# Kernel optimization log

Measured on AMD Instinct MI355X. Metric: run time of the kernel, lower is better.

Reference implementation:

```python
import jax, jax.numpy as jnp
import numpy as np

B, T, D, DH, DFF = 4, 2048, 1024, 1024, 4096


def setup_inputs() -> dict:
    key = jax.random.key(0)
    ks = jax.random.split(key, 8)
    s = 0.02
    return {
        "x": jax.random.normal(ks[0], (B, T, D), jnp.float32),
        "ln1_g": jnp.ones((D,), jnp.float32),
        "ln1_b": jnp.zeros((D,), jnp.float32),
        "W_q": jax.random.normal(ks[1], (D, DH), jnp.float32) * s,
        "b_q": jnp.zeros((DH,), jnp.float32),
        "W_k": jax.random.normal(ks[2], (D, DH), jnp.float32) * s,
        "b_k": jnp.zeros((DH,), jnp.float32),
        "W_v": jax.random.normal(ks[3], (D, DH), jnp.float32) * s,
        "b_v": jnp.zeros((DH,), jnp.float32),
        "ln2_g": jnp.ones((D,), jnp.float32),
        "ln2_b": jnp.zeros((D,), jnp.float32),
        "W_in": jax.random.normal(ks[4], (D, DFF), jnp.float32) * s,
        "b_in": jnp.zeros((DFF,), jnp.float32),
        "W_out": jax.random.normal(ks[5], (DFF, D), jnp.float32) * s,
        "b_out": jnp.zeros((D,), jnp.float32),
    }


def _layernorm(x, g, b, eps=1e-5):
    mu = jnp.mean(x, axis=-1, keepdims=True)
    var = jnp.var(x, axis=-1, keepdims=True)
    return (x - mu) * jax.lax.rsqrt(var + eps) * g + b


def reference(x, ln1_g, ln1_b, W_q, b_q, W_k, b_k, W_v, b_v,
              ln2_g, ln2_b, W_in, b_in, W_out, b_out):
    # --- attention branch (pre-LN) ---
    h = _layernorm(x, ln1_g, ln1_b)                      # [B,T,D]
    Q = h @ W_q + b_q                                    # [B,T,DH]
    K = h @ W_k + b_k
    V = h @ W_v + b_v
    scale = 1.0 / jnp.sqrt(jnp.asarray(K.shape[-1], h.dtype))
    att = jnp.einsum("btd,bsd->bts", Q, K) * scale       # [B,T,T]
    # NOTE: source calls att.masked_fill(...) without assignment -> mask
    # is discarded; faithfully no causal mask applied here.
    att = jax.nn.softmax(att, axis=-1)
    attn_out = jnp.einsum("bts,bsd->btd", att, V)        # [B,T,DH]
    x = x + attn_out
    # --- MLP branch (pre-LN) ---
    h2 = _layernorm(x, ln2_g, ln2_b)
    ff = jax.nn.gelu(h2 @ W_in + b_in, approximate=False)
    x = x + (ff @ W_out + b_out)
    return x
```

## Files before the change

### kernel.cpp

```cpp
#include <hip/hip_runtime.h>
#include <hip/hip_bf16.h>

#define B_    4
#define T_    2048
#define D_    1024
#define DH_   1024
#define DFF_  4096
#define MTOT  (B_ * T_)

using f32x4  = __attribute__((ext_vector_type(4))) float;
using bf16x8 = __attribute__((ext_vector_type(8))) short;

__device__ __forceinline__ unsigned short f2bf(float f) {
    unsigned u = __builtin_bit_cast(unsigned, f);
    u += 0x7fffu + ((u >> 16) & 1u);
    return (unsigned short)(u >> 16);
}

__device__ __forceinline__ void gload16(const short* g, short* l) {
    __builtin_amdgcn_global_load_lds(
        (const __attribute__((address_space(1))) unsigned int*)g,
        (__attribute__((address_space(3))) unsigned int*)l, 16, 0, 0);
}

__global__ __launch_bounds__(256) void transp_f32_bf16(
    const float* __restrict__ src, short* __restrict__ dst, int K, int N) {
    __shared__ float tile[32][33];
    int tk = blockIdx.y * 32, tn = blockIdx.x * 32;
    int tx = threadIdx.x & 31, ty = threadIdx.x >> 5;
#pragma unroll
    for (int i = 0; i < 4; i++) {
        int r = ty + i * 8;
        tile[r][tx] = src[(size_t)(tk + r) * N + tn + tx];
    }
    __syncthreads();
#pragma unroll
    for (int i = 0; i < 4; i++) {
        int r = ty + i * 8;
        dst[(size_t)(tn + r) * K + tk + tx] = f2bf(tile[tx][r]);
    }
}

__global__ void copyv(const float* __restrict__ s, float* __restrict__ d, int n) {
    int i = blockIdx.x * blockDim.x + threadIdx.x;
    if (i < n) d[i] = s[i];
}

__global__ __launch_bounds__(256) void ln_rows(
    const float* __restrict__ x, const float* __restrict__ g,
    const float* __restrict__ bta, short* __restrict__ out) {
    int row = blockIdx.x;
    const float* xr = x + (size_t)row * D_;
    int t = threadIdx.x;
    float4 v = *(const float4*)(xr + t * 4);
    float s  = v.x + v.y + v.z + v.w;
    float s2 = v.x * v.x + v.y * v.y + v.z * v.z + v.w * v.w;
#pragma unroll
    for (int off = 1; off < 64; off <<= 1) {
        s  += __shfl_xor(s, off);
        s2 += __shfl_xor(s2, off);
    }
    __shared__ float as_[4], as2_[4];
    int wave = t >> 6, lane = t & 63;
    if (lane == 0) { as_[wave] = s; as2_[wave] = s2; }
    __syncthreads();
    s  = as_[0] + as_[1] + as_[2] + as_[3];
    s2 = as2_[0] + as2_[1] + as2_[2] + as2_[3];
    float mean = s * (1.0f / D_);
    float var  = s2 * (1.0f / D_) - mean * mean;
    float rstd = rsqrtf(var + 1e-5f);
    float4 gv = *(const float4*)(g + t * 4);
    float4 bv = *(const float4*)(bta + t * 4);
    short4 o;
    o.x = f2bf((v.x - mean) * rstd * gv.x + bv.x);
    o.y = f2bf((v.y - mean) * rstd * gv.y + bv.y);
    o.z = f2bf((v.z - mean) * rstd * gv.z + bv.z);
    o.w = f2bf((v.w - mean) * rstd * gv.w + bv.w);
    *(short4*)(out + (size_t)row * D_ + t * 4) = o;
}

__global__ __launch_bounds__(256) void softmax_rows(float* __restrict__ S) {
    size_t row = blockIdx.x;
    float* sr = S + row * (size_t)T_;
    int t = threadIdx.x;
    float4 v0 = *(const float4*)(sr + t * 4);
    float4 v1 = *(const float4*)(sr + 1024 + t * 4);
    const float c = 0.03125f;
    float vv[8] = {v0.x * c, v0.y * c, v0.z * c, v0.w * c,
                   v1.x * c, v1.y * c, v1.z * c, v1.w * c};
    float mx = -1e30f;
#pragma unroll
    for (int i = 0; i < 8; i++) mx = fmaxf(mx, vv[i]);
#pragma unroll
    for (int off = 1; off < 64; off <<= 1) mx = fmaxf(mx, __shfl_xor(mx, off));
    __shared__ float sm_[4], ss[4];
    int wave = t >> 6, lane = t & 63;
    if (lane == 0) sm_[wave] = mx;
    __syncthreads();
    mx = fmaxf(fmaxf(sm_[0], sm_[1]), fmaxf(sm_[2], sm_[3]));
    float sum = 0.f;
#pragma unroll
    for (int i = 0; i < 8; i++) { vv[i] = expf(vv[i] - mx); sum += vv[i]; }
#pragma unroll
    for (int off = 1; off < 64; off <<= 1) sum += __shfl_xor(sum, off);
    if (lane == 0) ss[wave] = sum;
    __syncthreads();
    sum = ss[0] + ss[1] + ss[2] + ss[3];
    float inv = 1.0f / sum;
    short* pr = (short*)sr;
    short4 oa, ob;
    oa.x = f2bf(vv[0] * inv); oa.y = f2bf(vv[1] * inv);
    oa.z = f2bf(vv[2] * inv); oa.w = f2bf(vv[3] * inv);
    ob.x = f2bf(vv[4] * inv); ob.y = f2bf(vv[5] * inv);
    ob.z = f2bf(vv[6] * inv); ob.w = f2bf(vv[7] * inv);
    *(short4*)(pr + t * 4) = oa;
    *(short4*)(pr + 1024 + t * 4) = ob;
}

#define SLOT 8192
template<int BIAS_MODE, int ACT, int RES, int OUT_BF16>
__global__ __launch_bounds__(512, 2) void gemm8(
    const short* __restrict__ A, int lda, long long sA,
    const short* __restrict__ Bt, int ldb, long long sB,
    void* __restrict__ C, int ldc, long long sC,
    const float* __restrict__ bias,
    const float* __restrict__ res, int ldr, long long sR,
    int K) {
    extern __shared__ short smem_[];
    short* shA = smem_;
    short* shB = smem_ + 4 * SLOT;
    int z = blockIdx.z;
    int bm = blockIdx.y * 256, bn = blockIdx.x * 256;
    const short* gA = A  + (size_t)z * sA + (size_t)bm * lda;
    const short* gB = Bt + (size_t)z * sB + (size_t)bn * ldb;
    int tid = threadIdx.x, lane = tid & 63, w = tid >> 6;
    int wr = w >> 2, wc = w & 3;

    const short *pA0, *pA1, *pB0, *pB1;
    short *ldA0 = nullptr, *ldA1 = nullptr, *ldB0 = nullptr, *ldB1 = nullptr;
    {
        int o0 = tid * 16, o1 = (512 + tid) * 16;
        int s0 = o0 ^ (((o0 >> 7) & 3) << 4);
        int s1 = o1 ^ (((o1 >> 7) & 3) << 4);
        int r0 = s0 >> 6, c0 = (s0 & 63) >> 1;
        int r1 = s1 >> 6, c1 = (s1 & 63) >> 1;
        pA0 = gA + (size_t)r0 * lda + c0;
        pA1 = gA + (size_t)r1 * lda + c1;
        pB0 = gB + (size_t)r0 * ldb + c0;
        pB1 = gB + (size_t)r1 * ldb + c1;
        ldA0 = shA + tid * 8; ldA1 = shA + 4096 + tid * 8;
        ldB0 = shB + tid * 8; ldB1 = shB + 4096 + tid * 8;
    }
    int aoff[8], boff[4];
#pragma unroll
    for (int f = 0; f < 8; f++) {
        int b = (wr * 128 + f * 16 + (lane & 15)) * 64 + (lane >> 4) * 16;
        aoff[f] = b ^ (((b >> 7) & 3) << 4);
    }
#pragma unroll
    for (int f = 0; f < 4; f++) {
        int b = (wc * 64 + f * 16 + (lane & 15)) * 64 + (lane >> 4) * 16;
        boff[f] = b ^ (((b >> 7) & 3) << 4);
    }

    int nk = K >> 5;
    f32x4 acc[8][4] = {};

    gload16(pA0,      ldA0);          gload16(pA1,      ldA1);
    gload16(pB0,      ldB0);          gload16(pB1,      ldB1);
    gload16(pA0 + 32, ldA0 + SLOT);   gload16(pA1 + 32, ldA1 + SLOT);
    gload16(pB0 + 32, ldB0 + SLOT);   gload16(pB1 + 32, ldB1 + SLOT);
    asm volatile("s_waitcnt vmcnt(4)" ::: "memory");
    __builtin_amdgcn_s_barrier();

    for (int t = 0; t < nk; t++) {
        const char* sA_ = (const char*)(shA + (t & 3) * SLOT);
        const char* sB_ = (const char*)(shB + (t & 3) * SLOT);
        int e  = (t + 2) & 3;
        int ks = (t + 2 < nk ? t + 2 : nk - 1) * 32;
        bf16x8 a0 = *(const bf16x8*)(sA_ + aoff[0]);
        bf16x8 a1 = *(const bf16x8*)(sA_ + aoff[1]);
        bf16x8 a2 = *(const bf16x8*)(sA_ + aoff[2]);
        bf16x8 a3 = *(const bf16x8*)(sA_ + aoff[3]);
        bf16x8 b0 = *(const bf16x8*)(sB_ + boff[0]);
        bf16x8 b1 = *(const bf16x8*)(sB_ + boff[1]);
        bf16x8 b2 = *(const bf16x8*)(sB_ + boff[2]);
        bf16x8 b3 = *(const bf16x8*)(sB_ + boff[3]);
        gload16(pA0 + ks, shA + e * SLOT + tid * 8);
        gload16(pA1 + ks, shA + e * SLOT + 4096 + tid * 8);
        __builtin_amdgcn_s_barrier();
        asm volatile("s_waitcnt lgkmcnt(0)" ::: "memory");
        __builtin_amdgcn_sched_barrier(0);
        __builtin_amdgcn_s_setprio(1);
#define MF(r, av) \
        acc[r][0] = __builtin_amdgcn_mfma_f32_16x16x32_bf16(av, b0, acc[r][0], 0, 0, 0); \
        acc[r][1] = __builtin_amdgcn_mfma_f32_16x16x32_bf16(av, b1, acc[r][1], 0, 0, 0); \
        acc[r][2] = __builtin_amdgcn_mfma_f32_16x16x32_bf16(av, b2, acc[r][2], 0, 0, 0); \
        acc[r][3] = __builtin_amdgcn_mfma_f32_16x16x32_bf16(av, b3, acc[r][3], 0, 0, 0);
        MF(0, a0) MF(1, a1) MF(2, a2) MF(3, a3)
        __builtin_amdgcn_s_setprio(0);
        __builtin_amdgcn_s_barrier();
        a0 = *(const bf16x8*)(sA_ + aoff[4]);
        a1 = *(const bf16x8*)(sA_ + aoff[5]);
        a2 = *(const bf16x8*)(sA_ + aoff[6]);
        a3 = *(const bf16x8*)(sA_ + aoff[7]);
        gload16(pB0 + ks, shB + e * SLOT + tid * 8);
        gload16(pB1 + ks, shB + e * SLOT + 4096 + tid * 8);
        asm volatile("s_waitcnt vmcnt(4)" ::: "memory");
        __builtin_amdgcn_s_barrier();
        asm volatile("s_waitcnt lgkmcnt(0)" ::: "memory");
        __builtin_amdgcn_sched_barrier(0);
        __builtin_amdgcn_s_setprio(1);
        MF(4, a0) MF(5, a1) MF(6, a2) MF(7, a3)
#undef MF
        __builtin_amdgcn_s_setprio(0);
        __builtin_amdgcn_s_barrier();
    }
    asm volatile("s_waitcnt vmcnt(0)" ::: "memory");

    size_t zc = (size_t)z * (size_t)sC;
#pragma unroll
    for (int fr = 0; fr < 8; fr++) {
#pragma unroll
        for (int fn = 0; fn < 4; fn++) {
            int col = bn + wc * 64 + fn * 16 + (lane & 15);
#pragma unroll
            for (int r = 0; r < 4; r++) {
                int row = bm + wr * 128 + fr * 16 + (lane >> 4) * 4 + r;
                float v = acc[fr][fn][r];
                if (BIAS_MODE == 1) v += bias[col];
                else if (BIAS_MODE == 2) v += bias[row];
                if (ACT == 1) v = 0.5f * v * (1.0f + erff(v * 0.70710678118654752f));
                if (RES) v += res[(size_t)z * sR + (size_t)row * ldr + col];
                if (OUT_BF16) ((short*)C)[zc + (size_t)row * ldc + col] = f2bf(v);
                else          ((float*)C)[zc + (size_t)row * ldc + col] = v;
            }
        }
    }
}

#define SHBYTES (8 * SLOT * 2)

extern "C" void kernel_launch(void* const* d_in, const int* in_sizes, int n_in,
                              void* d_out, int out_size, void* d_ws, size_t ws_size,
                              hipStream_t stream) {
    const float* x    = (const float*)d_in[0];
    const float* ln1g = (const float*)d_in[1];
    const float* ln1b = (const float*)d_in[2];
    const float* Wq   = (const float*)d_in[3];
    const float* bq   = (const float*)d_in[4];
    const float* Wk   = (const float*)d_in[5];
    const float* bk   = (const float*)d_in[6];
    const float* Wv   = (const float*)d_in[7];
    const float* bv   = (const float*)d_in[8];
    const float* ln2g = (const float*)d_in[9];
    const float* ln2b = (const float*)d_in[10];
    const float* Win  = (const float*)d_in[11];
    const float* bin  = (const float*)d_in[12];
    const float* Wout = (const float*)d_in[13];
    const float* bout = (const float*)d_in[14];

    char* ws = (char*)d_ws;
    size_t off = 0;
    auto alloc = [&](size_t bytes) {
        void* p = ws + off;
        off += (bytes + 255) & ~(size_t)255;
        return p;
    };
    short* WqkT  = (short*)alloc((size_t)2048 * 1024 * 2);
    short* WvT   = (short*)alloc((size_t)1024 * 1024 * 2);
    short* WinT  = (short*)alloc((size_t)4096 * 1024 * 2);
    short* WoutT = (short*)alloc((size_t)1024 * 4096 * 2);
    float* bqk   = (float*)alloc((size_t)2048 * 4);
    short* h     = (short*)alloc((size_t)MTOT * 1024 * 2);
    short* QK    = (short*)alloc((size_t)MTOT * 2048 * 2);
    short* VT    = (short*)alloc((size_t)1024 * 8192 * 2);
    float* S     = (float*)alloc((size_t)4 * 2048 * 2048 * 4);
    float* x1    = (float*)alloc((size_t)MTOT * 1024 * 4);
    (void)ws_size; (void)in_sizes; (void)n_in; (void)out_size;

    hipFuncSetAttribute((const void*)gemm8<1,0,0,1>, hipFuncAttributeMaxDynamicSharedMemorySize, SHBYTES);
    hipFuncSetAttribute((const void*)gemm8<2,0,0,1>, hipFuncAttributeMaxDynamicSharedMemorySize, SHBYTES);
    hipFuncSetAttribute((const void*)gemm8<0,0,0,0>, hipFuncAttributeMaxDynamicSharedMemorySize, SHBYTES);
    hipFuncSetAttribute((const void*)gemm8<0,0,1,0>, hipFuncAttributeMaxDynamicSharedMemorySize, SHBYTES);
    hipFuncSetAttribute((const void*)gemm8<1,1,0,1>, hipFuncAttributeMaxDynamicSharedMemorySize, SHBYTES);
    hipFuncSetAttribute((const void*)gemm8<1,0,1,0>, hipFuncAttributeMaxDynamicSharedMemorySize, SHBYTES);

    transp_f32_bf16<<<dim3(32, 32), 256, 0, stream>>>(Wq, WqkT, 1024, 1024);
    transp_f32_bf16<<<dim3(32, 32), 256, 0, stream>>>(Wk, WqkT + (size_t)1024 * 1024, 1024, 1024);
    transp_f32_bf16<<<dim3(32, 32), 256, 0, stream>>>(Wv, WvT, 1024, 1024);
    transp_f32_bf16<<<dim3(128, 32), 256, 0, stream>>>(Win, WinT, 1024, 4096);
    transp_f32_bf16<<<dim3(32, 128), 256, 0, stream>>>(Wout, WoutT, 4096, 1024);
    copyv<<<4, 256, 0, stream>>>(bq, bqk, 1024);
    copyv<<<4, 256, 0, stream>>>(bk, bqk + 1024, 1024);

    ln_rows<<<MTOT, 256, 0, stream>>>(x, ln1g, ln1b, h);

    gemm8<1, 0, 0, 1><<<dim3(8, 32, 1), 512, SHBYTES, stream>>>(
        h, 1024, 0, WqkT, 1024, 0, QK, 2048, 0, bqk, nullptr, 0, 0, 1024);

    gemm8<2, 0, 0, 1><<<dim3(32, 4, 1), 512, SHBYTES, stream>>>(
        WvT, 1024, 0, h, 1024, 0, VT, 8192, 0, bv, nullptr, 0, 0, 1024);

    gemm8<0, 0, 0, 0><<<dim3(8, 8, 4), 512, SHBYTES, stream>>>(
        QK, 2048, 4194304LL, QK + 1024, 2048, 4194304LL,
        S, 2048, 4194304LL, nullptr, nullptr, 0, 0, 1024);

    softmax_rows<<<MTOT, 256, 0, stream>>>(S);

    gemm8<0, 0, 1, 0><<<dim3(4, 8, 4), 512, SHBYTES, stream>>>(
        (short*)S, 4096, 8388608LL, VT, 8192, 2048LL,
        x1, 1024, 2097152LL, nullptr, x, 1024, 2097152LL, 2048);

    ln_rows<<<MTOT, 256, 0, stream>>>(x1, ln2g, ln2b, h);

    short* ff = (short*)S;
    gemm8<1, 1, 0, 1><<<dim3(16, 32, 1), 512, SHBYTES, stream>>>(
        h, 1024, 0, WinT, 1024, 0, ff, 4096, 0, bin, nullptr, 0, 0, 1024);

    gemm8<1, 0, 1, 0><<<dim3(4, 32, 1), 512, SHBYTES, stream>>>(
        ff, 4096, 0, WoutT, 4096, 0, (float*)d_out, 1024, 0, bout,
        x1, 1024, 0, 4096);
}
```

Before: 464.0 us.

## Deepen GEMM prefetch to three stages and remap workgroups per XCD

```diff
diff --git a/kernel.cpp b/kernel.cpp
--- a/kernel.cpp
+++ b/kernel.cpp
@@ -129,15 +129,22 @@
     extern __shared__ short smem_[];
     short* shA = smem_;
     short* shB = smem_ + 4 * SLOT;
-    int z = blockIdx.z;
-    int bm = blockIdx.y * 256, bn = blockIdx.x * 256;
+
+    int gx = gridDim.x, gy = gridDim.y;
+    int nwg = gx * gy * gridDim.z;
+    int lid = blockIdx.x + gx * (blockIdx.y + gy * blockIdx.z);
+    int q = nwg >> 3, r = nwg & 7, xcd = lid & 7, i_ = lid >> 3;
+    int nid = (xcd < r ? xcd * (q + 1) : r * (q + 1) + (xcd - r) * q) + i_;
+    int bx = nid % gx; int tmp_ = nid / gx; int by = tmp_ % gy; int z = tmp_ / gy;
+
+    int bm = by * 256, bn = bx * 256;
     const short* gA = A  + (size_t)z * sA + (size_t)bm * lda;
     const short* gB = Bt + (size_t)z * sB + (size_t)bn * ldb;
     int tid = threadIdx.x, lane = tid & 63, w = tid >> 6;
     int wr = w >> 2, wc = w & 3;
 
     const short *pA0, *pA1, *pB0, *pB1;
-    short *ldA0 = nullptr, *ldA1 = nullptr, *ldB0 = nullptr, *ldB1 = nullptr;
+    short *ldA0, *ldA1, *ldB0, *ldB1;
     {
         int o0 = tid * 16, o1 = (512 + tid) * 16;
         int s0 = o0 ^ (((o0 >> 7) & 3) << 4);
@@ -166,18 +173,19 @@
     int nk = K >> 5;
     f32x4 acc[8][4] = {};
 
-    gload16(pA0,      ldA0);          gload16(pA1,      ldA1);
-    gload16(pB0,      ldB0);          gload16(pB1,      ldB1);
-    gload16(pA0 + 32, ldA0 + SLOT);   gload16(pA1 + 32, ldA1 + SLOT);
-    gload16(pB0 + 32, ldB0 + SLOT);   gload16(pB1 + 32, ldB1 + SLOT);
-    asm volatile("s_waitcnt vmcnt(4)" ::: "memory");
+#pragma unroll
+    for (int s = 0; s < 3; s++) {
+        gload16(pA0 + s * 32, ldA0 + s * SLOT);  gload16(pA1 + s * 32, ldA1 + s * SLOT);
+        gload16(pB0 + s * 32, ldB0 + s * SLOT);  gload16(pB1 + s * 32, ldB1 + s * SLOT);
+    }
+    asm volatile("s_waitcnt vmcnt(8)" ::: "memory");
     __builtin_amdgcn_s_barrier();
 
     for (int t = 0; t < nk; t++) {
         const char* sA_ = (const char*)(shA + (t & 3) * SLOT);
         const char* sB_ = (const char*)(shB + (t & 3) * SLOT);
-        int e  = (t + 2) & 3;
-        int ks = (t + 2 < nk ? t + 2 : nk - 1) * 32;
+        int e  = (t + 3) & 3;
+        int ks = (t + 3 < nk ? t + 3 : nk - 1) * 32;
         bf16x8 a0 = *(const bf16x8*)(sA_ + aoff[0]);
         bf16x8 a1 = *(const bf16x8*)(sA_ + aoff[1]);
         bf16x8 a2 = *(const bf16x8*)(sA_ + aoff[2]);
@@ -192,11 +200,11 @@
         asm volatile("s_waitcnt lgkmcnt(0)" ::: "memory");
         __builtin_amdgcn_sched_barrier(0);
         __builtin_amdgcn_s_setprio(1);
-#define MF(r, av) \
-        acc[r][0] = __builtin_amdgcn_mfma_f32_16x16x32_bf16(av, b0, acc[r][0], 0, 0, 0); \
-        acc[r][1] = __builtin_amdgcn_mfma_f32_16x16x32_bf16(av, b1, acc[r][1], 0, 0, 0); \
-        acc[r][2] = __builtin_amdgcn_mfma_f32_16x16x32_bf16(av, b2, acc[r][2], 0, 0, 0); \
-        acc[r][3] = __builtin_amdgcn_mfma_f32_16x16x32_bf16(av, b3, acc[r][3], 0, 0, 0);
+#define MF(r_, av) \
+        acc[r_][0] = __builtin_amdgcn_mfma_f32_16x16x32_bf16(av, b0, acc[r_][0], 0, 0, 0); \
+        acc[r_][1] = __builtin_amdgcn_mfma_f32_16x16x32_bf16(av, b1, acc[r_][1], 0, 0, 0); \
+        acc[r_][2] = __builtin_amdgcn_mfma_f32_16x16x32_bf16(av, b2, acc[r_][2], 0, 0, 0); \
+        acc[r_][3] = __builtin_amdgcn_mfma_f32_16x16x32_bf16(av, b3, acc[r_][3], 0, 0, 0);
         MF(0, a0) MF(1, a1) MF(2, a2) MF(3, a3)
         __builtin_amdgcn_s_setprio(0);
         __builtin_amdgcn_s_barrier();
@@ -206,7 +214,7 @@
         a3 = *(const bf16x8*)(sA_ + aoff[7]);
         gload16(pB0 + ks, shB + e * SLOT + tid * 8);
         gload16(pB1 + ks, shB + e * SLOT + 4096 + tid * 8);
-        asm volatile("s_waitcnt vmcnt(4)" ::: "memory");
+        asm volatile("s_waitcnt vmcnt(8)" ::: "memory");
         __builtin_amdgcn_s_barrier();
         asm volatile("s_waitcnt lgkmcnt(0)" ::: "memory");
         __builtin_amdgcn_sched_barrier(0);
@@ -225,9 +233,9 @@
         for (int fn = 0; fn < 4; fn++) {
             int col = bn + wc * 64 + fn * 16 + (lane & 15);
 #pragma unroll
-            for (int r = 0; r < 4; r++) {
-                int row = bm + wr * 128 + fr * 16 + (lane >> 4) * 4 + r;
-                float v = acc[fr][fn][r];
+            for (int r_ = 0; r_ < 4; r_++) {
+                int row = bm + wr * 128 + fr * 16 + (lane >> 4) * 4 + r_;
+                float v = acc[fr][fn][r_];
                 if (BIAS_MODE == 1) v += bias[col];
                 else if (BIAS_MODE == 2) v += bias[row];
                 if (ACT == 1) v = 0.5f * v * (1.0f + erff(v * 0.70710678118654752f));
```

Result: faster. 454.9 us (-2.0%).
